# Kernel optimization log

Measured on AMD Instinct MI355X. Metric: run time of the kernel, lower is better.

The kernel has to match this reference:

```python
import jax, jax.numpy as jnp
import numpy as np

N_NODES = 100000
N_EDGES = 1600000
IN_FEAT = 256
OUT_FEAT = 128


def setup_inputs() -> dict:
    key = jax.random.key(0)
    ks = jax.random.split(key, 8)
    x = jax.random.normal(ks[0], (N_NODES, IN_FEAT), dtype=jnp.float32)
    rows0 = jnp.sort(jax.random.randint(ks[1], (N_EDGES,), 0, N_NODES, dtype=jnp.int32))
    cols0 = jax.random.randint(ks[2], (N_EDGES,), 0, N_NODES, dtype=jnp.int32)
    vals0 = jax.random.uniform(ks[3], (N_EDGES,), dtype=jnp.float32)
    rows1 = jnp.sort(jax.random.randint(ks[4], (N_EDGES,), 0, N_NODES, dtype=jnp.int32))
    cols1 = jax.random.randint(ks[5], (N_EDGES,), 0, N_NODES, dtype=jnp.int32)
    vals1 = jax.random.uniform(ks[6], (N_EDGES,), dtype=jnp.float32)
    kw0, kw1 = jax.random.split(ks[7])
    # glorot-uniform-ish scale for [IN_FEAT, OUT_FEAT]
    limit = float(np.sqrt(6.0 / (IN_FEAT + OUT_FEAT)))
    W0 = jax.random.uniform(kw0, (IN_FEAT, OUT_FEAT), minval=-limit, maxval=limit, dtype=jnp.float32)
    W1 = jax.random.uniform(kw1, (IN_FEAT, OUT_FEAT), minval=-limit, maxval=limit, dtype=jnp.float32)
    return {"x": x, "rows0": rows0, "cols0": cols0, "vals0": vals0,
            "rows1": rows1, "cols1": cols1, "vals1": vals1, "W0": W0, "W1": W1}


def _spmm(rows, cols, vals, dense, n_rows):
    # sparse [N,N] (COO) @ dense [N,D] -> [N,D]
    gathered = vals[:, None] * dense[cols]          # [E, D]
    return jax.ops.segment_sum(gathered, rows, num_segments=n_rows)


def reference(x, rows0, cols0, vals0, rows1, cols1, vals1, W0, W1):
    # GraphConvolution with dropout=0 (identity), featureless=False, no bias, relu.
    # support_i = A_i @ (x @ W_i); output = relu(sum_i support_i)
    s0 = _spmm(rows0, cols0, vals0, x @ W0, N_NODES)
    s1 = _spmm(rows1, cols1, vals1, x @ W1, N_NODES)
    return jax.nn.relu(s0 + s1)
```

## Files before the change

kernel.cpp:

```cpp
#include <hip/hip_runtime.h>
#include <hip/hip_bf16.h>
#include <stdint.h>

#define NN   100000
#define NE   1600000
#define KIN  256
#define FOUT 128

typedef __attribute__((ext_vector_type(8))) short short8;
typedef __attribute__((ext_vector_type(4))) float f32x4;
typedef __attribute__((ext_vector_type(2))) float f32x2;

static __device__ __forceinline__ unsigned short f2bf(float f) {
  unsigned int u = __float_as_uint(f);
  u += 0x7fffu + ((u >> 16) & 1u);
  return (unsigned short)(u >> 16);
}

static __device__ __forceinline__ short8 pack8(float4 u, float4 v) {
  short8 r;
  r[0] = (short)f2bf(u.x); r[1] = (short)f2bf(u.y);
  r[2] = (short)f2bf(u.z); r[3] = (short)f2bf(u.w);
  r[4] = (short)f2bf(v.x); r[5] = (short)f2bf(v.y);
  r[6] = (short)f2bf(v.z); r[7] = (short)f2bf(v.w);
  return r;
}

__global__ void convert_w(const float* __restrict__ W0, const float* __restrict__ W1,
                          unsigned short* __restrict__ wt) {
  int n = blockIdx.x;
  int k = threadIdx.x;
  int which = blockIdx.y;
  const float* W = which ? W1 : W0;
  wt[(size_t)which * (FOUT * KIN) + n * KIN + k] = f2bf(W[k * FOUT + n]);
}

__global__ __launch_bounds__(256) void build_rowptr(const int* __restrict__ rows0,
                                                    const int* __restrict__ rows1,
                                                    int* __restrict__ rp0,
                                                    int* __restrict__ rp1) {
  const int e = blockIdx.x * 256 + threadIdx.x;
  const int* rows = blockIdx.y ? rows1 : rows0;
  int* rp = blockIdx.y ? rp1 : rp0;
  int r1 = rows[e];
  int r2 = (e + 1 < NE) ? rows[e + 1] : NN;
  if (e == 0)
    for (int r = 0; r <= r1; ++r) rp[r] = 0;
  for (int r = r1 + 1; r <= r2; ++r) rp[r] = e + 1;
}

__global__ __launch_bounds__(256) void gemm_mfma(const float* __restrict__ x,
                                                 const unsigned short* __restrict__ wt,
                                                 unsigned short* __restrict__ h) {
  __shared__ __align__(16) unsigned short tile[4][32 * 64];

  const int tid  = threadIdx.x;
  const int lane = tid & 63;
  const int wv   = tid >> 6;
  const int which = blockIdx.y;
  const int rowbase = blockIdx.x * 64 + (wv >> 1) * 32;
  const int colbase = (wv & 1) * 64;
  const int m    = lane & 15;
  const int quad = lane >> 4;

  const unsigned short* w = wt + (size_t)which * (FOUT * KIN);
  unsigned short* hh = h + (size_t)which * NN * FOUT;

  int r0 = rowbase + m;
  int r1 = rowbase + 16 + m;
  int r0c = r0 < NN ? r0 : NN - 1;
  int r1c = r1 < NN ? r1 : NN - 1;
  const float* ap0 = x + (size_t)r0c * KIN + quad * 8;
  const float* ap1 = x + (size_t)r1c * KIN + quad * 8;
  const unsigned short* b0p = w + (size_t)(colbase + 0  + m) * KIN + quad * 8;
  const unsigned short* b1p = w + (size_t)(colbase + 16 + m) * KIN + quad * 8;
  const unsigned short* b2p = w + (size_t)(colbase + 32 + m) * KIN + quad * 8;
  const unsigned short* b3p = w + (size_t)(colbase + 48 + m) * KIN + quad * 8;

  f32x4 acc[2][4];
#pragma unroll
  for (int i = 0; i < 2; ++i)
#pragma unroll
    for (int j = 0; j < 4; ++j)
      acc[i][j] = (f32x4){0.f, 0.f, 0.f, 0.f};

#pragma unroll 2
  for (int ko = 0; ko < KIN; ko += 32) {
    float4 a0lo = *(const float4*)(ap0 + ko);
    float4 a0hi = *(const float4*)(ap0 + ko + 4);
    float4 a1lo = *(const float4*)(ap1 + ko);
    float4 a1hi = *(const float4*)(ap1 + ko + 4);
    short8 b0 = *(const short8*)(b0p + ko);
    short8 b1 = *(const short8*)(b1p + ko);
    short8 b2 = *(const short8*)(b2p + ko);
    short8 b3 = *(const short8*)(b3p + ko);
    short8 a0 = pack8(a0lo, a0hi);
    short8 a1 = pack8(a1lo, a1hi);
    acc[0][0] = __builtin_amdgcn_mfma_f32_16x16x32_bf16(a0, b0, acc[0][0], 0, 0, 0);
    acc[0][1] = __builtin_amdgcn_mfma_f32_16x16x32_bf16(a0, b1, acc[0][1], 0, 0, 0);
    acc[0][2] = __builtin_amdgcn_mfma_f32_16x16x32_bf16(a0, b2, acc[0][2], 0, 0, 0);
    acc[0][3] = __builtin_amdgcn_mfma_f32_16x16x32_bf16(a0, b3, acc[0][3], 0, 0, 0);
    acc[1][0] = __builtin_amdgcn_mfma_f32_16x16x32_bf16(a1, b0, acc[1][0], 0, 0, 0);
    acc[1][1] = __builtin_amdgcn_mfma_f32_16x16x32_bf16(a1, b1, acc[1][1], 0, 0, 0);
    acc[1][2] = __builtin_amdgcn_mfma_f32_16x16x32_bf16(a1, b2, acc[1][2], 0, 0, 0);
    acc[1][3] = __builtin_amdgcn_mfma_f32_16x16x32_bf16(a1, b3, acc[1][3], 0, 0, 0);
  }

#pragma unroll
  for (int i = 0; i < 2; ++i)
#pragma unroll
    for (int reg = 0; reg < 4; ++reg)
#pragma unroll
      for (int j = 0; j < 4; ++j)
        tile[wv][(i * 16 + quad * 4 + reg) * 64 + j * 16 + m] = f2bf(acc[i][j][reg]);

#pragma unroll
  for (int p = 0; p < 4; ++p) {
    int row = p * 8 + (lane >> 3);
    int colb = (lane & 7) * 8;
    uint4 v = *(const uint4*)&tile[wv][row * 64 + colb];
    int grow = rowbase + row;
    if (grow < NN)
      *(uint4*)&hh[(size_t)grow * FOUT + colbase + colb] = v;
  }
}

static __device__ __forceinline__ void consume8(const float* __restrict__ vals, int i,
                                                const unsigned* g, float& sx, float& sy) {
#pragma unroll
  for (int u = 0; u < 8; ++u) {
    float v = vals[i + u];
    sx += v * __uint_as_float(g[u] << 16);
    sy += v * __uint_as_float(g[u] & 0xffff0000u);
  }
}

static __device__ __forceinline__ void tail_spmm(const int* __restrict__ cols,
                                                 const float* __restrict__ vals,
                                                 const unsigned short* __restrict__ hsrc,
                                                 int i, int e, int fo,
                                                 float& sx, float& sy) {
  for (; i + 4 <= e; i += 4) {
    int c0 = cols[i], c1 = cols[i + 1], c2 = cols[i + 2], c3 = cols[i + 3];
    unsigned g0 = *(const unsigned*)(hsrc + (size_t)c0 * FOUT + fo);
    unsigned g1 = *(const unsigned*)(hsrc + (size_t)c1 * FOUT + fo);
    unsigned g2 = *(const unsigned*)(hsrc + (size_t)c2 * FOUT + fo);
    unsigned g3 = *(const unsigned*)(hsrc + (size_t)c3 * FOUT + fo);
    float v0 = vals[i], v1 = vals[i + 1], v2 = vals[i + 2], v3 = vals[i + 3];
    sx += v0 * __uint_as_float(g0 << 16);
    sy += v0 * __uint_as_float(g0 & 0xffff0000u);
    sx += v1 * __uint_as_float(g1 << 16);
    sy += v1 * __uint_as_float(g1 & 0xffff0000u);
    sx += v2 * __uint_as_float(g2 << 16);
    sy += v2 * __uint_as_float(g2 & 0xffff0000u);
    sx += v3 * __uint_as_float(g3 << 16);
    sy += v3 * __uint_as_float(g3 & 0xffff0000u);
  }
  for (; i < e; ++i) {
    int c = cols[i];
    float v = vals[i];
    unsigned g = *(const unsigned*)(hsrc + (size_t)c * FOUT + fo);
    sx += v * __uint_as_float(g << 16);
    sy += v * __uint_as_float(g & 0xffff0000u);
  }
}

__global__ __launch_bounds__(256) void spmm_relu(
    const int* __restrict__ rp0, const int* __restrict__ cols0, const float* __restrict__ vals0,
    const int* __restrict__ rp1, const int* __restrict__ cols1, const float* __restrict__ vals1,
    const unsigned short* __restrict__ h, float* __restrict__ out) {
  const int lane = threadIdx.x & 63;
  int r = blockIdx.x * 4 + (threadIdx.x >> 6);
  r = __builtin_amdgcn_readfirstlane(r);
  const int fo = lane * 2;

  const unsigned short* h0 = h;
  const unsigned short* h1 = h + (size_t)NN * FOUT;

  int i0 = __builtin_amdgcn_readfirstlane(rp0[r]);
  int e0 = __builtin_amdgcn_readfirstlane(rp0[r + 1]);
  int i1 = __builtin_amdgcn_readfirstlane(rp1[r]);
  int e1 = __builtin_amdgcn_readfirstlane(rp1[r + 1]);

  float sx = 0.f, sy = 0.f;

  while (i0 + 8 <= e0 && i1 + 8 <= e1) {
    unsigned g0[8], g1[8];
#pragma unroll
    for (int u = 0; u < 8; ++u) {
      int c = cols0[i0 + u];
      g0[u] = *(const unsigned*)(h0 + (size_t)c * FOUT + fo);
    }
#pragma unroll
    for (int u = 0; u < 8; ++u) {
      int c = cols1[i1 + u];
      g1[u] = *(const unsigned*)(h1 + (size_t)c * FOUT + fo);
    }
    consume8(vals0, i0, g0, sx, sy);
    consume8(vals1, i1, g1, sx, sy);
    i0 += 8;
    i1 += 8;
  }
  tail_spmm(cols0, vals0, h0, i0, e0, fo, sx, sy);
  tail_spmm(cols1, vals1, h1, i1, e1, fo, sx, sy);

  f32x2 o;
  o.x = sx > 0.f ? sx : 0.f;
  o.y = sy > 0.f ? sy : 0.f;
  __builtin_nontemporal_store(o, (f32x2*)(out + (size_t)r * FOUT + fo));
}

extern "C" void kernel_launch(void* const* d_in, const int* in_sizes, int n_in,
                              void* d_out, int out_size, void* d_ws, size_t ws_size,
                              hipStream_t stream) {
  const float* x     = (const float*)d_in[0];
  const int*   rows0 = (const int*)d_in[1];
  const int*   cols0 = (const int*)d_in[2];
  const float* vals0 = (const float*)d_in[3];
  const int*   rows1 = (const int*)d_in[4];
  const int*   cols1 = (const int*)d_in[5];
  const float* vals1 = (const float*)d_in[6];
  const float* W0    = (const float*)d_in[7];
  const float* W1    = (const float*)d_in[8];
  float* out = (float*)d_out;

  char* ws = (char*)d_ws;
  unsigned short* wt = (unsigned short*)(ws);
  unsigned short* h  = (unsigned short*)(ws + 131072);
  int* rp0 = (int*)(ws + 51331072);
  int* rp1 = (int*)(ws + 51731136);

  build_rowptr<<<dim3(6250, 2), 256, 0, stream>>>(rows0, rows1, rp0, rp1);
  convert_w<<<dim3(128, 2), 256, 0, stream>>>(W0, W1, wt);
  gemm_mfma<<<dim3((NN + 63) / 64, 2), 256, 0, stream>>>(x, wt, h);
  spmm_relu<<<25000, 256, 0, stream>>>(rp0, cols0, vals0, rp1, cols1, vals1, h, out);
}
```

Baseline: 386.2 us.

## Fuse setup kernels, share x tile across both weights, double-buffer SpMM gathers

```diff
diff --git a/kernel.cpp b/kernel.cpp
--- a/kernel.cpp
+++ b/kernel.cpp
@@ -26,27 +26,30 @@
   return r;
 }
 
-__global__ void convert_w(const float* __restrict__ W0, const float* __restrict__ W1,
-                          unsigned short* __restrict__ wt) {
-  int n = blockIdx.x;
-  int k = threadIdx.x;
-  int which = blockIdx.y;
-  const float* W = which ? W1 : W0;
-  wt[(size_t)which * (FOUT * KIN) + n * KIN + k] = f2bf(W[k * FOUT + n]);
-}
-
-__global__ __launch_bounds__(256) void build_rowptr(const int* __restrict__ rows0,
-                                                    const int* __restrict__ rows1,
-                                                    int* __restrict__ rp0,
-                                                    int* __restrict__ rp1) {
-  const int e = blockIdx.x * 256 + threadIdx.x;
-  const int* rows = blockIdx.y ? rows1 : rows0;
-  int* rp = blockIdx.y ? rp1 : rp0;
-  int r1 = rows[e];
-  int r2 = (e + 1 < NE) ? rows[e + 1] : NN;
-  if (e == 0)
-    for (int r = 0; r <= r1; ++r) rp[r] = 0;
-  for (int r = r1 + 1; r <= r2; ++r) rp[r] = e + 1;
+__global__ __launch_bounds__(256) void setup(const int* __restrict__ rows0,
+                                             const int* __restrict__ rows1,
+                                             const float* __restrict__ W0,
+                                             const float* __restrict__ W1,
+                                             int* __restrict__ rp0,
+                                             int* __restrict__ rp1,
+                                             unsigned short* __restrict__ wt) {
+  const int which = blockIdx.y;
+  const int bx = blockIdx.x;
+  if (bx < 6250) {
+    const int e = bx * 256 + threadIdx.x;
+    const int* rows = which ? rows1 : rows0;
+    int* rp = which ? rp1 : rp0;
+    int r1 = rows[e];
+    int r2 = (e + 1 < NE) ? rows[e + 1] : NN;
+    if (e == 0)
+      for (int r = 0; r <= r1; ++r) rp[r] = 0;
+    for (int r = r1 + 1; r <= r2; ++r) rp[r] = e + 1;
+  } else {
+    const int n = bx - 6250;
+    const int k = threadIdx.x;
+    const float* W = which ? W1 : W0;
+    wt[(size_t)which * (FOUT * KIN) + n * KIN + k] = f2bf(W[k * FOUT + n]);
+  }
 }
 
 __global__ __launch_bounds__(256) void gemm_mfma(const float* __restrict__ x,
@@ -57,21 +60,17 @@
   const int tid  = threadIdx.x;
   const int lane = tid & 63;
   const int wv   = tid >> 6;
-  const int which = blockIdx.y;
-  const int rowbase = blockIdx.x * 64 + (wv >> 1) * 32;
+  const int which = wv >> 1;
   const int colbase = (wv & 1) * 64;
+  const int rowbase = blockIdx.x * 32;
   const int m    = lane & 15;
   const int quad = lane >> 4;
 
   const unsigned short* w = wt + (size_t)which * (FOUT * KIN);
   unsigned short* hh = h + (size_t)which * NN * FOUT;
 
-  int r0 = rowbase + m;
-  int r1 = rowbase + 16 + m;
-  int r0c = r0 < NN ? r0 : NN - 1;
-  int r1c = r1 < NN ? r1 : NN - 1;
-  const float* ap0 = x + (size_t)r0c * KIN + quad * 8;
-  const float* ap1 = x + (size_t)r1c * KIN + quad * 8;
+  const float* ap0 = x + (size_t)(rowbase + m) * KIN + quad * 8;
+  const float* ap1 = x + (size_t)(rowbase + 16 + m) * KIN + quad * 8;
   const unsigned short* b0p = w + (size_t)(colbase + 0  + m) * KIN + quad * 8;
   const unsigned short* b1p = w + (size_t)(colbase + 16 + m) * KIN + quad * 8;
   const unsigned short* b2p = w + (size_t)(colbase + 32 + m) * KIN + quad * 8;
@@ -119,9 +118,17 @@
     int row = p * 8 + (lane >> 3);
     int colb = (lane & 7) * 8;
     uint4 v = *(const uint4*)&tile[wv][row * 64 + colb];
-    int grow = rowbase + row;
-    if (grow < NN)
-      *(uint4*)&hh[(size_t)grow * FOUT + colbase + colb] = v;
+    *(uint4*)&hh[(size_t)(rowbase + row) * FOUT + colbase + colb] = v;
+  }
+}
+
+static __device__ __forceinline__ void issue8(const int* __restrict__ cols, int i,
+                                              const unsigned short* __restrict__ hsrc,
+                                              int fo, unsigned* g) {
+#pragma unroll
+  for (int u = 0; u < 8; ++u) {
+    int c = cols[i + u];
+    g[u] = *(const unsigned*)(hsrc + (size_t)c * FOUT + fo);
   }
 }
 
@@ -165,6 +172,41 @@
   }
 }
 
+static __device__ __forceinline__ void spmm_pipe(const int* __restrict__ cols,
+                                                 const float* __restrict__ vals,
+                                                 const unsigned short* __restrict__ hsrc,
+                                                 const int* __restrict__ rp,
+                                                 int r, int fo,
+                                                 float& sx, float& sy) {
+  int i = __builtin_amdgcn_readfirstlane(rp[r]);
+  int e = __builtin_amdgcn_readfirstlane(rp[r + 1]);
+  if (i + 8 <= e) {
+    unsigned gA[8], gB[8];
+    issue8(cols, i, hsrc, fo, gA);
+    for (;;) {
+      if (i + 16 <= e) {
+        issue8(cols, i + 8, hsrc, fo, gB);
+        consume8(vals, i, gA, sx, sy);
+        i += 8;
+      } else {
+        consume8(vals, i, gA, sx, sy);
+        i += 8;
+        break;
+      }
+      if (i + 16 <= e) {
+        issue8(cols, i + 8, hsrc, fo, gA);
+        consume8(vals, i, gB, sx, sy);
+        i += 8;
+      } else {
+        consume8(vals, i, gB, sx, sy);
+        i += 8;
+        break;
+      }
+    }
+  }
+  tail_spmm(cols, vals, hsrc, i, e, fo, sx, sy);
+}
+
 __global__ __launch_bounds__(256) void spmm_relu(
     const int* __restrict__ rp0, const int* __restrict__ cols0, const float* __restrict__ vals0,
     const int* __restrict__ rp1, const int* __restrict__ cols1, const float* __restrict__ vals1,
@@ -177,32 +219,9 @@
   const unsigned short* h0 = h;
   const unsigned short* h1 = h + (size_t)NN * FOUT;
 
-  int i0 = __builtin_amdgcn_readfirstlane(rp0[r]);
-  int e0 = __builtin_amdgcn_readfirstlane(rp0[r + 1]);
-  int i1 = __builtin_amdgcn_readfirstlane(rp1[r]);
-  int e1 = __builtin_amdgcn_readfirstlane(rp1[r + 1]);
-
   float sx = 0.f, sy = 0.f;
-
-  while (i0 + 8 <= e0 && i1 + 8 <= e1) {
-    unsigned g0[8], g1[8];
-#pragma unroll
-    for (int u = 0; u < 8; ++u) {
-      int c = cols0[i0 + u];
-      g0[u] = *(const unsigned*)(h0 + (size_t)c * FOUT + fo);
-    }
-#pragma unroll
-    for (int u = 0; u < 8; ++u) {
-      int c = cols1[i1 + u];
-      g1[u] = *(const unsigned*)(h1 + (size_t)c * FOUT + fo);
-    }
-    consume8(vals0, i0, g0, sx, sy);
-    consume8(vals1, i1, g1, sx, sy);
-    i0 += 8;
-    i1 += 8;
-  }
-  tail_spmm(cols0, vals0, h0, i0, e0, fo, sx, sy);
-  tail_spmm(cols1, vals1, h1, i1, e1, fo, sx, sy);
+  spmm_pipe(cols0, vals0, h0, rp0, r, fo, sx, sy);
+  spmm_pipe(cols1, vals1, h1, rp1, r, fo, sx, sy);
 
   f32x2 o;
   o.x = sx > 0.f ? sx : 0.f;
@@ -230,8 +249,7 @@
   int* rp0 = (int*)(ws + 51331072);
   int* rp1 = (int*)(ws + 51731136);
 
-  build_rowptr<<<dim3(6250, 2), 256, 0, stream>>>(rows0, rows1, rp0, rp1);
-  convert_w<<<dim3(128, 2), 256, 0, stream>>>(W0, W1, wt);
-  gemm_mfma<<<dim3((NN + 63) / 64, 2), 256, 0, stream>>>(x, wt, h);
-  spmm_relu<<<25000, 256, 0, stream>>>(rp0, cols0, vals0, rp1, cols1, vals1, h, out);
-}
+  setup<<<dim3(6378, 2), 256, 0, stream>>>(rows0, rows1, W0, W1, rp0, rp1, wt);
+  gemm_mfma<<<NN / 32, 256, 0, stream>>>(x, wt, h);
+  spmm_relu<<<NN / 4, 256, 0, stream>>>(rp0, cols0, vals0, rp1, cols1, vals1, h, out);
+}
```

After: 397.9 us. 1.03x slower.
